# Kernel tuning notes

Measured on AMD Instinct MI355X. Metric: run time of the kernel, lower is better.

The kernel has to match this reference:

```python
import jax, jax.numpy as jnp
import numpy as np


def setup_inputs() -> dict:
    key = jax.random.key(0)
    k1, k2, k3, k4 = jax.random.split(key, 4)
    S, D, DKQ, DV = 8192, 2048, 128, 128
    x = jax.random.normal(k1, (S, D), dtype=jnp.float32)
    w_q = jax.random.uniform(k2, (D, DKQ), dtype=jnp.float32)
    w_k = jax.random.uniform(k3, (D, DKQ), dtype=jnp.float32)
    w_v = jax.random.uniform(k4, (D, DV), dtype=jnp.float32)
    return {"x": x, "w_q": w_q, "w_k": w_k, "w_v": w_v}


def reference(x, w_q, w_k, w_v):
    # x: [S, D]; single-head causal attention, unbatched as in the source.
    dim_kq = w_q.shape[1]
    q = x @ w_q  # [S, DKQ]
    k = x @ w_k  # [S, DKQ]
    v = x @ w_v  # [S, DV]
    scores = (q @ k.T) / jnp.sqrt(jnp.asarray(dim_kq, q.dtype))  # [S, S]
    S = scores.shape[0]
    causal = jnp.tril(jnp.ones((S, S), dtype=bool))
    scores = jnp.where(causal, scores, -jnp.inf)
    att_w = jax.nn.softmax(scores, axis=-1)
    return att_w @ v  # [S, DV]
```

## Files before the change

kernel.cpp:

```cpp
#include <hip/hip_runtime.h>

#define S_LEN 8192
#define D_DIM 2048
#define HD    128
#define KVB   32
#define NCH   8

typedef __attribute__((ext_vector_type(8))) short bf16x8;
typedef __attribute__((ext_vector_type(4))) float f32x4;

__device__ __forceinline__ unsigned short f2bf(float f) {
  unsigned int u = __float_as_uint(f);
  u += 0x7fffu + ((u >> 16) & 1u);
  return (unsigned short)(u >> 16);
}
__device__ __forceinline__ float bf2f(unsigned short h) {
  return __uint_as_float(((unsigned int)h) << 16);
}

__device__ __forceinline__ void glds16(const void* g, const short* l) {
  __builtin_amdgcn_global_load_lds(
      (const __attribute__((address_space(1))) void*)g,
      (__attribute__((address_space(3))) void*)l, 16, 0, 0);
}

__global__ __launch_bounds__(256)
void split_x_kernel(const float* __restrict__ x,
                    unsigned short* __restrict__ xh, unsigned short* __restrict__ xl)
{
  const size_t n4 = (size_t)S_LEN * D_DIM / 4;
  size_t idx = (size_t)blockIdx.x * 256 + threadIdx.x;
  const size_t stride = (size_t)gridDim.x * 256;
  for (; idx < n4; idx += stride) {
    float4 v = ((const float4*)x)[idx];
    ushort4 h, l;
#pragma unroll
    for (int j = 0; j < 4; ++j) {
      float f = ((const float*)&v)[j];
      unsigned short hb = f2bf(f);
      ((unsigned short*)&h)[j] = hb;
      ((unsigned short*)&l)[j] = f2bf(f - bf2f(hb));
    }
    ((ushort4*)xh)[idx] = h;
    ((ushort4*)xl)[idx] = l;
  }
}

__global__ __launch_bounds__(256)
void split_w_kernel(const float* __restrict__ wq, const float* __restrict__ wk,
                    const float* __restrict__ wv,
                    unsigned short* __restrict__ wTh, unsigned short* __restrict__ wTl)
{
  const int mode = blockIdx.y;
  const float* __restrict__ w = (mode == 0) ? wq : (mode == 1) ? wk : wv;
  unsigned short* __restrict__ oh = wTh + (size_t)mode * HD * D_DIM;
  unsigned short* __restrict__ ol = wTl + (size_t)mode * HD * D_DIM;
  const int k0 = blockIdx.x * 64;

  __shared__ float ws[64][132];
  const int t = threadIdx.x;
#pragma unroll
  for (int i = 0; i < 8; ++i) {
    int idx = t + i * 256;
    int row = idx >> 5;
    int c4  = idx & 31;
    *(float4*)&ws[row][c4 * 4] = *(const float4*)(w + (size_t)(k0 + row) * HD + c4 * 4);
  }
  __syncthreads();
#pragma unroll
  for (int i = 0; i < 4; ++i) {
    int task = t + i * 256;
    int col = task >> 3;
    int kc  = task & 7;
    ushort4 h[2], l[2];
#pragma unroll
    for (int e = 0; e < 8; ++e) {
      float f = ws[kc * 8 + e][col];
      unsigned short hb = f2bf(f);
      ((unsigned short*)&h[e >> 2])[e & 3] = hb;
      ((unsigned short*)&l[e >> 2])[e & 3] = f2bf(f - bf2f(hb));
    }
    size_t off = (size_t)col * D_DIM + k0 + kc * 8;
    *(ushort4*)(oh + off)     = h[0];
    *(ushort4*)(oh + off + 4) = h[1];
    *(ushort4*)(ol + off)     = l[0];
    *(ushort4*)(ol + off + 4) = l[1];
  }
}

__global__ __launch_bounds__(256)
void proj_kernel(const unsigned short* __restrict__ xh, const unsigned short* __restrict__ xl,
                 const unsigned short* __restrict__ wTh, const unsigned short* __restrict__ wTl,
                 unsigned short* __restrict__ q_hi, unsigned short* __restrict__ q_lo,
                 unsigned short* __restrict__ k_hi, unsigned short* __restrict__ k_lo,
                 unsigned short* __restrict__ vT)
{
  __shared__ short sm[2][12288];

  const int mode = blockIdx.y;
  const int mt   = blockIdx.x;
  const bool split = (mode < 2);

  const unsigned short* gxh = xh + (size_t)mt * 64 * D_DIM;
  const unsigned short* gxl = xl + (size_t)mt * 64 * D_DIM;
  const unsigned short* gwh = wTh + (size_t)mode * HD * D_DIM;
  const unsigned short* gwl = wTl + (size_t)mode * HD * D_DIM;

  const int t   = threadIdx.x;
  const int wid = t >> 6;
  const int ln  = t & 63;
  const int cl  = ln & 15;
  const int g4  = ln >> 4;

  auto stage = [&](int kt, int buf) {
    short* b = sm[buf];
    {
      int slot = wid * 64 + ln;
      int row = slot >> 2, sc = slot & 3;
      int kof = (sc ^ (row & 3)) * 8;
      glds16(gxh + (size_t)row * D_DIM + kt + kof, b + wid * 512);
      if (split)
        glds16(gxl + (size_t)row * D_DIM + kt + kof, b + 2048 + wid * 512);
    }
#pragma unroll
    for (int g = 0; g < 2; ++g) {
      int slot = g * 256 + wid * 64 + ln;
      int col = slot >> 2, sc = slot & 3;
      int kof = (sc ^ (col & 3)) * 8;
      glds16(gwh + (size_t)col * D_DIM + kt + kof, b + 4096 + (g * 256 + wid * 64) * 8);
      if (split)
        glds16(gwl + (size_t)col * D_DIM + kt + kof, b + 8192 + (g * 256 + wid * 64) * 8);
    }
  };

  f32x4 acc[2][4];
#pragma unroll
  for (int m = 0; m < 2; ++m)
#pragma unroll
    for (int n = 0; n < 4; ++n) acc[m][n] = f32x4{0.f, 0.f, 0.f, 0.f};

  stage(0, 0);
  __syncthreads();

  for (int kt = 0, step = 0; kt < D_DIM; kt += 32, ++step) {
    const int cur = step & 1;
    if (kt + 32 < D_DIM) stage(kt + 32, cur ^ 1);

    const short* b = sm[cur];
    bf16x8 a_h[2], a_l[2], b_h[4], b_l[4];
#pragma unroll
    for (int m = 0; m < 2; ++m) {
      int row = (wid >> 1) * 32 + m * 16 + cl;
      int byte = row * 64 + ((g4 ^ (row & 3)) << 4);
      a_h[m] = *(const bf16x8*)((const char*)b + byte);
      if (split) a_l[m] = *(const bf16x8*)((const char*)b + 4096 + byte);
    }
#pragma unroll
    for (int n = 0; n < 4; ++n) {
      int col = (wid & 1) * 64 + n * 16 + cl;
      int byte = col * 64 + ((g4 ^ (col & 3)) << 4);
      b_h[n] = *(const bf16x8*)((const char*)b + 8192 + byte);
      if (split) b_l[n] = *(const bf16x8*)((const char*)b + 16384 + byte);
    }

#pragma unroll
    for (int m = 0; m < 2; ++m)
#pragma unroll
      for (int n = 0; n < 4; ++n)
        acc[m][n] = __builtin_amdgcn_mfma_f32_16x16x32_bf16(a_h[m], b_h[n], acc[m][n], 0, 0, 0);
    if (split) {
#pragma unroll
      for (int m = 0; m < 2; ++m)
#pragma unroll
        for (int n = 0; n < 4; ++n) {
          acc[m][n] = __builtin_amdgcn_mfma_f32_16x16x32_bf16(a_l[m], b_h[n], acc[m][n], 0, 0, 0);
          acc[m][n] = __builtin_amdgcn_mfma_f32_16x16x32_bf16(a_h[m], b_l[n], acc[m][n], 0, 0, 0);
        }
    }
    __syncthreads();
  }

  const int rbase = mt * 64 + (wid >> 1) * 32 + g4 * 4;
  const int cbase = (wid & 1) * 64 + cl;

  if (mode < 2) {
    const float scale = (mode == 0) ? 0.08838834764831843f : 1.0f;
    unsigned short* __restrict__ oh = (mode == 0) ? q_hi : k_hi;
    unsigned short* __restrict__ ol = (mode == 0) ? q_lo : k_lo;
#pragma unroll
    for (int m = 0; m < 2; ++m)
#pragma unroll
      for (int n = 0; n < 4; ++n)
#pragma unroll
        for (int r = 0; r < 4; ++r) {
          float val = acc[m][n][r] * scale;
          unsigned short hb = f2bf(val);
          size_t off = (size_t)(rbase + m * 16 + r) * HD + cbase + n * 16;
          oh[off] = hb;
          ol[off] = f2bf(val - bf2f(hb));
        }
  } else {
#pragma unroll
    for (int m = 0; m < 2; ++m)
#pragma unroll
      for (int n = 0; n < 4; ++n) {
        ushort4 o;
#pragma unroll
        for (int r = 0; r < 4; ++r) ((unsigned short*)&o)[r] = f2bf(acc[m][n][r]);
        int col = cbase + n * 16;
        *(ushort4*)(vT + (size_t)col * S_LEN + rbase + m * 16) = o;
      }
  }
}

__global__ __launch_bounds__(256, 3)
void attn_kernel(const unsigned short* __restrict__ q_hi, const unsigned short* __restrict__ q_lo,
                 const unsigned short* __restrict__ k_hi, const unsigned short* __restrict__ k_lo,
                 const unsigned short* __restrict__ vT,
                 float* __restrict__ part_o, float* __restrict__ part_ml)
{
  __shared__ short ls_kh[2][4096];
  __shared__ short ls_kl[2][4096];
  __shared__ short ls_v [2][4096];
  __shared__ short ls_p [4][640];

  const int t   = threadIdx.x;
  const int wid = t >> 6;
  const int ln  = t & 63;
  const int cl  = ln & 15;
  const int g4  = ln >> 4;
  const int pairId = blockIdx.x >> 3;
  const int chunk  = blockIdx.x & 7;

  short* pw = ls_p[wid];

  auto stage = [&](int j, int buf) {
    const unsigned short* gkh = k_hi + (size_t)j * KVB * HD;
    const unsigned short* gkl = k_lo + (size_t)j * KVB * HD;
    const unsigned short* gv  = vT + (size_t)j * KVB;
#pragma unroll
    for (int i = 0; i < 2; ++i) {
      int slot = wid * 128 + i * 64 + ln;
      int row = slot >> 4, sc = slot & 15;
      int c16 = sc ^ (row & 7);
      glds16(gkh + row * HD + c16 * 8, &ls_kh[buf][(wid * 128 + i * 64) * 8]);
      glds16(gkl + row * HD + c16 * 8, &ls_kl[buf][(wid * 128 + i * 64) * 8]);
    }
#pragma unroll
    for (int i = 0; i < 2; ++i) {
      int slot = wid * 128 + i * 64 + ln;
      int d = slot >> 2, sub = slot & 3;
      int s2 = sub ^ ((d >> 1) & 3);
      glds16(gv + (size_t)d * S_LEN + s2 * 8, &ls_v[buf][(wid * 128 + i * 64) * 8]);
    }
  };

  for (int hh = 0; hh < 2; ++hh) {
    const int T = hh ? (127 - pairId) : pairId;
    const int jmaxB = T * 2 + 1;
    const int jmaxW = T * 2 + (wid >> 1);
    const int rowbase = T * 64 + wid * 16;

    bf16x8 qh[4], ql[4];
    {
      const size_t qoff = ((size_t)rowbase + cl) * HD + g4 * 8;
#pragma unroll
      for (int kc = 0; kc < 4; ++kc) {
        qh[kc] = *(const bf16x8*)(q_hi + qoff + kc * 32);
        ql[kc] = *(const bf16x8*)(q_lo + qoff + kc * 32);
      }
    }

    float m_i[4], l_i[4];
    f32x4 o_acc[8];
#pragma unroll
    for (int i = 0; i < 4; ++i) { m_i[i] = -1e30f; l_i[i] = 0.f; }
#pragma unroll
    for (int c = 0; c < 8; ++c) o_acc[c] = f32x4{0.f, 0.f, 0.f, 0.f};

    if (chunk <= jmaxB) {
      int cur = 0;
      stage(chunk, 0);
      __syncthreads();
      for (int j = chunk; j <= jmaxB; j += NCH) {
        if (j + NCH <= jmaxB) stage(j + NCH, cur ^ 1);

        if (j <= jmaxW) {
          f32x4 s[2];
          s[0] = f32x4{0.f, 0.f, 0.f, 0.f};
          s[1] = f32x4{0.f, 0.f, 0.f, 0.f};
#pragma unroll
          for (int kc = 0; kc < 4; ++kc) {
#pragma unroll
            for (int c = 0; c < 2; ++c) {
              const int kcol = c * 16 + cl;
              const int byte = kcol * 256 + ((((kc << 2) + g4) ^ (kcol & 7)) << 4);
              bf16x8 khf = *(const bf16x8*)((const char*)ls_kh[cur] + byte);
              bf16x8 klf = *(const bf16x8*)((const char*)ls_kl[cur] + byte);
              s[c] = __builtin_amdgcn_mfma_f32_16x16x32_bf16(qh[kc], khf, s[c], 0, 0, 0);
              s[c] = __builtin_amdgcn_mfma_f32_16x16x32_bf16(ql[kc], khf, s[c], 0, 0, 0);
              s[c] = __builtin_amdgcn_mfma_f32_16x16x32_bf16(qh[kc], klf, s[c], 0, 0, 0);
            }
          }

          if (j * KVB + KVB - 1 > rowbase) {
#pragma unroll
            for (int c = 0; c < 2; ++c)
#pragma unroll
              for (int i = 0; i < 4; ++i) {
                int col = j * KVB + c * 16 + cl;
                int row = rowbase + g4 * 4 + i;
                if (col > row) s[c][i] = -1e30f;
              }
          }

          bool ok = true;
#pragma unroll
          for (int i = 0; i < 4; ++i) {
            float mx = fmaxf(s[0][i], s[1][i]);
            ok = ok && (mx <= m_i[i] + 8.0f);
          }
          if (!__all(ok)) {
#pragma unroll
            for (int i = 0; i < 4; ++i) {
              float rm = fmaxf(s[0][i], s[1][i]);
              rm = fmaxf(rm, __shfl_xor(rm, 1));
              rm = fmaxf(rm, __shfl_xor(rm, 2));
              rm = fmaxf(rm, __shfl_xor(rm, 4));
              rm = fmaxf(rm, __shfl_xor(rm, 8));
              float mnew = fmaxf(m_i[i], rm);
              float corr = __expf(m_i[i] - mnew);
              l_i[i] *= corr;
#pragma unroll
              for (int c2 = 0; c2 < 8; ++c2) o_acc[c2][i] *= corr;
              m_i[i] = mnew;
            }
          }

#pragma unroll
          for (int c = 0; c < 2; ++c)
#pragma unroll
            for (int i = 0; i < 4; ++i) {
              float sv = s[c][i];
              float p = (sv > -1e29f) ? __expf(sv - m_i[i]) : 0.f;
              l_i[i] += p;
              pw[(g4 * 4 + i) * 40 + c * 16 + cl] = (short)f2bf(p);
            }

          bf16x8 pa = *(const bf16x8*)((const char*)pw + cl * 80 + g4 * 16);
#pragma unroll
          for (int c2 = 0; c2 < 8; ++c2) {
            const int d = c2 * 16 + cl;
            const int byte = d * 64 + (((g4 ^ ((d >> 1) & 3))) << 4);
            bf16x8 vb = *(const bf16x8*)((const char*)ls_v[cur] + byte);
            o_acc[c2] = __builtin_amdgcn_mfma_f32_16x16x32_bf16(pa, vb, o_acc[c2], 0, 0, 0);
          }
        }

        __syncthreads();
        cur ^= 1;
      }
    }

    const int base = T * NCH + chunk;
#pragma unroll
    for (int c2 = 0; c2 < 8; ++c2)
#pragma unroll
      for (int i = 0; i < 4; ++i)
        part_o[((size_t)base * 64 + wid * 16 + g4 * 4 + i) * HD + c2 * 16 + cl] = o_acc[c2][i];

#pragma unroll
    for (int i = 0; i < 4; ++i) {
      float lv = l_i[i];
      lv += __shfl_xor(lv, 1);
      lv += __shfl_xor(lv, 2);
      lv += __shfl_xor(lv, 4);
      lv += __shfl_xor(lv, 8);
      if (cl == 0) {
        int rl = wid * 16 + g4 * 4 + i;
        part_ml[base * 128 + rl]      = m_i[i];
        part_ml[base * 128 + 64 + rl] = lv;
      }
    }
  }
}

__global__ __launch_bounds__(128)
void merge_kernel(const float* __restrict__ part_o, const float* __restrict__ part_ml,
                  float* __restrict__ out)
{
  const int row = blockIdx.x;
  const int T   = row >> 6;
  const int r   = row & 63;
  const int c   = threadIdx.x;

  float m[NCH], l[NCH];
  float mstar = -3e38f;
#pragma unroll
  for (int s = 0; s < NCH; ++s) {
    m[s] = part_ml[(T * NCH + s) * 128 + r];
    l[s] = part_ml[(T * NCH + s) * 128 + 64 + r];
    mstar = fmaxf(mstar, m[s]);
  }
  float num = 0.f, den = 0.f;
#pragma unroll
  for (int s = 0; s < NCH; ++s) {
    float wgt = __expf(m[s] - mstar);
    den += l[s] * wgt;
    num += wgt * part_o[((size_t)(T * NCH + s) * 64 + r) * HD + c];
  }
  out[(size_t)row * HD + c] = num / den;
}

extern "C" void kernel_launch(void* const* d_in, const int* in_sizes, int n_in,
                              void* d_out, int out_size, void* d_ws, size_t ws_size,
                              hipStream_t stream)
{
  const float* x  = (const float*)d_in[0];
  const float* wq = (const float*)d_in[1];
  const float* wk = (const float*)d_in[2];
  const float* wv = (const float*)d_in[3];
  float* out = (float*)d_out;

  unsigned short* p = (unsigned short*)d_ws;
  unsigned short* xh = p;  p += (size_t)S_LEN * D_DIM;
  unsigned short* xl = p;  p += (size_t)S_LEN * D_DIM;
  unsigned short* wTh = p; p += (size_t)3 * HD * D_DIM;
  unsigned short* wTl = p; p += (size_t)3 * HD * D_DIM;
  unsigned short* q_hi = p; p += (size_t)S_LEN * HD;
  unsigned short* q_lo = p; p += (size_t)S_LEN * HD;
  unsigned short* k_hi = p; p += (size_t)S_LEN * HD;
  unsigned short* k_lo = p; p += (size_t)S_LEN * HD;
  unsigned short* vT   = p; p += (size_t)S_LEN * HD;
  float* part_o  = (float*)xh;
  float* part_ml = (float*)xl;

  split_x_kernel<<<4096, 256, 0, stream>>>(x, xh, xl);
  split_w_kernel<<<dim3(32, 3), 256, 0, stream>>>(wq, wk, wv, wTh, wTl);
  proj_kernel<<<dim3(128, 3), 256, 0, stream>>>(xh, xl, wTh, wTl,
                                                q_hi, q_lo, k_hi, k_lo, vT);
  attn_kernel<<<dim3(512), 256, 0, stream>>>(q_hi, q_lo, k_hi, k_lo, vT,
                                             part_o, part_ml);
  merge_kernel<<<dim3(8192), 128, 0, stream>>>(part_o, part_ml, out);
}
```

Before: 151.1 us.

## Switch attention to 32x32 MFMA tiles with 128-row blocks and 16 KV chunks

Restructures the attention kernel so each wave owns 32 query rows and uses 32x32x16 bf16 MFMAs instead of 16x16x32. Query tiles grow to 128 rows per block, and the KV split count rises from 8 to 16 to keep the grid size the same. Each K/V tile staged in LDS is now reused by more query rows, and fewer MFMA instructions are issued. In exchange, register pressure rises (launch bounds drop to 2 blocks per CU), the causal diagonal wastes more work, and the merge kernel must combine more partial results.

```diff
diff --git a/kernel.cpp b/kernel.cpp
--- a/kernel.cpp
+++ b/kernel.cpp
@@ -4,10 +4,11 @@
 #define D_DIM 2048
 #define HD    128
 #define KVB   32
-#define NCH   8
+#define NCH   16
 
 typedef __attribute__((ext_vector_type(8))) short bf16x8;
 typedef __attribute__((ext_vector_type(4))) float f32x4;
+typedef __attribute__((ext_vector_type(16))) float f32x16;
 
 __device__ __forceinline__ unsigned short f2bf(float f) {
   unsigned int u = __float_as_uint(f);
@@ -213,7 +214,7 @@
   }
 }
 
-__global__ __launch_bounds__(256, 3)
+__global__ __launch_bounds__(256, 2)
 void attn_kernel(const unsigned short* __restrict__ q_hi, const unsigned short* __restrict__ q_lo,
                  const unsigned short* __restrict__ k_hi, const unsigned short* __restrict__ k_lo,
                  const unsigned short* __restrict__ vT,
@@ -222,15 +223,15 @@
   __shared__ short ls_kh[2][4096];
   __shared__ short ls_kl[2][4096];
   __shared__ short ls_v [2][4096];
-  __shared__ short ls_p [4][640];
+  __shared__ short ls_p [4][32 * 40];
 
   const int t   = threadIdx.x;
   const int wid = t >> 6;
   const int ln  = t & 63;
-  const int cl  = ln & 15;
-  const int g4  = ln >> 4;
-  const int pairId = blockIdx.x >> 3;
-  const int chunk  = blockIdx.x & 7;
+  const int lc  = ln & 31;
+  const int l5  = ln >> 5;
+  const int pairId = blockIdx.x >> 4;
+  const int chunk  = blockIdx.x & 15;
 
   short* pw = ls_p[wid];
 
@@ -240,43 +241,43 @@
     const unsigned short* gv  = vT + (size_t)j * KVB;
 #pragma unroll
     for (int i = 0; i < 2; ++i) {
-      int slot = wid * 128 + i * 64 + ln;
+      int slot = i * 256 + t;
       int row = slot >> 4, sc = slot & 15;
       int c16 = sc ^ (row & 7);
-      glds16(gkh + row * HD + c16 * 8, &ls_kh[buf][(wid * 128 + i * 64) * 8]);
-      glds16(gkl + row * HD + c16 * 8, &ls_kl[buf][(wid * 128 + i * 64) * 8]);
+      glds16(gkh + row * HD + c16 * 8, &ls_kh[buf][slot * 8]);
+      glds16(gkl + row * HD + c16 * 8, &ls_kl[buf][slot * 8]);
     }
 #pragma unroll
     for (int i = 0; i < 2; ++i) {
-      int slot = wid * 128 + i * 64 + ln;
+      int slot = i * 256 + t;
       int d = slot >> 2, sub = slot & 3;
       int s2 = sub ^ ((d >> 1) & 3);
-      glds16(gv + (size_t)d * S_LEN + s2 * 8, &ls_v[buf][(wid * 128 + i * 64) * 8]);
+      glds16(gv + (size_t)d * S_LEN + s2 * 8, &ls_v[buf][slot * 8]);
     }
   };
 
   for (int hh = 0; hh < 2; ++hh) {
-    const int T = hh ? (127 - pairId) : pairId;
-    const int jmaxB = T * 2 + 1;
-    const int jmaxW = T * 2 + (wid >> 1);
-    const int rowbase = T * 64 + wid * 16;
-
-    bf16x8 qh[4], ql[4];
+    const int T = hh ? (63 - pairId) : pairId;
+    const int jmaxB = 4 * T + 3;
+    const int jmaxW = 4 * T + wid;
+    const int rowbase = T * 128 + wid * 32;
+
+    bf16x8 qh[8], ql[8];
     {
-      const size_t qoff = ((size_t)rowbase + cl) * HD + g4 * 8;
-#pragma unroll
-      for (int kc = 0; kc < 4; ++kc) {
-        qh[kc] = *(const bf16x8*)(q_hi + qoff + kc * 32);
-        ql[kc] = *(const bf16x8*)(q_lo + qoff + kc * 32);
+      const size_t qoff = ((size_t)rowbase + lc) * HD + l5 * 8;
+#pragma unroll
+      for (int ks = 0; ks < 8; ++ks) {
+        qh[ks] = *(const bf16x8*)(q_hi + qoff + ks * 16);
+        ql[ks] = *(const bf16x8*)(q_lo + qoff + ks * 16);
       }
     }
 
-    float m_i[4], l_i[4];
-    f32x4 o_acc[8];
-#pragma unroll
-    for (int i = 0; i < 4; ++i) { m_i[i] = -1e30f; l_i[i] = 0.f; }
-#pragma unroll
-    for (int c = 0; c < 8; ++c) o_acc[c] = f32x4{0.f, 0.f, 0.f, 0.f};
+    float m_i[16], l_i[16];
+    f32x16 o_acc[4];
+#pragma unroll
+    for (int r = 0; r < 16; ++r) { m_i[r] = -1e30f; l_i[r] = 0.f; }
+#pragma unroll
+    for (int ct = 0; ct < 4; ++ct) o_acc[ct] = f32x16{};
 
     if (chunk <= jmaxB) {
       int cur = 0;
@@ -286,74 +287,77 @@
         if (j + NCH <= jmaxB) stage(j + NCH, cur ^ 1);
 
         if (j <= jmaxW) {
-          f32x4 s[2];
-          s[0] = f32x4{0.f, 0.f, 0.f, 0.f};
-          s[1] = f32x4{0.f, 0.f, 0.f, 0.f};
-#pragma unroll
-          for (int kc = 0; kc < 4; ++kc) {
-#pragma unroll
-            for (int c = 0; c < 2; ++c) {
-              const int kcol = c * 16 + cl;
-              const int byte = kcol * 256 + ((((kc << 2) + g4) ^ (kcol & 7)) << 4);
-              bf16x8 khf = *(const bf16x8*)((const char*)ls_kh[cur] + byte);
-              bf16x8 klf = *(const bf16x8*)((const char*)ls_kl[cur] + byte);
-              s[c] = __builtin_amdgcn_mfma_f32_16x16x32_bf16(qh[kc], khf, s[c], 0, 0, 0);
-              s[c] = __builtin_amdgcn_mfma_f32_16x16x32_bf16(ql[kc], khf, s[c], 0, 0, 0);
-              s[c] = __builtin_amdgcn_mfma_f32_16x16x32_bf16(qh[kc], klf, s[c], 0, 0, 0);
+          f32x16 sa = f32x16{}, sb = f32x16{};
+#pragma unroll
+          for (int ks = 0; ks < 4; ++ks) {
+            const int ch = ks * 2 + l5;
+            const int byteK = lc * 256 + ((ch ^ (lc & 7)) << 4);
+            bf16x8 khf = *(const bf16x8*)((const char*)ls_kh[cur] + byteK);
+            bf16x8 klf = *(const bf16x8*)((const char*)ls_kl[cur] + byteK);
+            sa = __builtin_amdgcn_mfma_f32_32x32x16_bf16(qh[ks], khf, sa, 0, 0, 0);
+            sa = __builtin_amdgcn_mfma_f32_32x32x16_bf16(ql[ks], khf, sa, 0, 0, 0);
+            sa = __builtin_amdgcn_mfma_f32_32x32x16_bf16(qh[ks], klf, sa, 0, 0, 0);
+          }
+#pragma unroll
+          for (int ks = 4; ks < 8; ++ks) {
+            const int ch = ks * 2 + l5;
+            const int byteK = lc * 256 + ((ch ^ (lc & 7)) << 4);
+            bf16x8 khf = *(const bf16x8*)((const char*)ls_kh[cur] + byteK);
+            bf16x8 klf = *(const bf16x8*)((const char*)ls_kl[cur] + byteK);
+            sb = __builtin_amdgcn_mfma_f32_32x32x16_bf16(qh[ks], khf, sb, 0, 0, 0);
+            sb = __builtin_amdgcn_mfma_f32_32x32x16_bf16(ql[ks], khf, sb, 0, 0, 0);
+            sb = __builtin_amdgcn_mfma_f32_32x32x16_bf16(qh[ks], klf, sb, 0, 0, 0);
+          }
+          f32x16 s = sa + sb;
+
+          if (j == jmaxW) {
+#pragma unroll
+            for (int r = 0; r < 16; ++r) {
+              int row = rowbase + (r & 3) + 8 * (r >> 2) + 4 * l5;
+              int col = j * KVB + lc;
+              if (col > row) s[r] = -1e30f;
             }
           }
 
-          if (j * KVB + KVB - 1 > rowbase) {
-#pragma unroll
-            for (int c = 0; c < 2; ++c)
-#pragma unroll
-              for (int i = 0; i < 4; ++i) {
-                int col = j * KVB + c * 16 + cl;
-                int row = rowbase + g4 * 4 + i;
-                if (col > row) s[c][i] = -1e30f;
-              }
-          }
-
           bool ok = true;
 #pragma unroll
-          for (int i = 0; i < 4; ++i) {
-            float mx = fmaxf(s[0][i], s[1][i]);
-            ok = ok && (mx <= m_i[i] + 8.0f);
-          }
+          for (int r = 0; r < 16; ++r) ok = ok && (s[r] <= m_i[r] + 8.0f);
           if (!__all(ok)) {
 #pragma unroll
-            for (int i = 0; i < 4; ++i) {
-              float rm = fmaxf(s[0][i], s[1][i]);
+            for (int r = 0; r < 16; ++r) {
+              float rm = s[r];
               rm = fmaxf(rm, __shfl_xor(rm, 1));
               rm = fmaxf(rm, __shfl_xor(rm, 2));
               rm = fmaxf(rm, __shfl_xor(rm, 4));
               rm = fmaxf(rm, __shfl_xor(rm, 8));
-              float mnew = fmaxf(m_i[i], rm);
-              float corr = __expf(m_i[i] - mnew);
-              l_i[i] *= corr;
-#pragma unroll
-              for (int c2 = 0; c2 < 8; ++c2) o_acc[c2][i] *= corr;
-              m_i[i] = mnew;
+              rm = fmaxf(rm, __shfl_xor(rm, 16));
+              float mnew = fmaxf(m_i[r], rm);
+              float corr = __expf(m_i[r] - mnew);
+              l_i[r] *= corr;
+#pragma unroll
+              for (int ct = 0; ct < 4; ++ct) o_acc[ct][r] *= corr;
+              m_i[r] = mnew;
             }
           }
 
 #pragma unroll
-          for (int c = 0; c < 2; ++c)
-#pragma unroll
-            for (int i = 0; i < 4; ++i) {
-              float sv = s[c][i];
-              float p = (sv > -1e29f) ? __expf(sv - m_i[i]) : 0.f;
-              l_i[i] += p;
-              pw[(g4 * 4 + i) * 40 + c * 16 + cl] = (short)f2bf(p);
-            }
-
-          bf16x8 pa = *(const bf16x8*)((const char*)pw + cl * 80 + g4 * 16);
-#pragma unroll
-          for (int c2 = 0; c2 < 8; ++c2) {
-            const int d = c2 * 16 + cl;
-            const int byte = d * 64 + (((g4 ^ ((d >> 1) & 3))) << 4);
-            bf16x8 vb = *(const bf16x8*)((const char*)ls_v[cur] + byte);
-            o_acc[c2] = __builtin_amdgcn_mfma_f32_16x16x32_bf16(pa, vb, o_acc[c2], 0, 0, 0);
+          for (int r = 0; r < 16; ++r) {
+            float sv = s[r];
+            float p = (sv > -1e29f) ? __expf(sv - m_i[r]) : 0.f;
+            l_i[r] += p;
+            pw[((r & 3) + 8 * (r >> 2) + 4 * l5) * 40 + lc] = (short)f2bf(p);
+          }
+
+          bf16x8 pa0 = *(const bf16x8*)((const char*)pw + lc * 80 + l5 * 16);
+          bf16x8 pa1 = *(const bf16x8*)((const char*)pw + lc * 80 + 32 + l5 * 16);
+#pragma unroll
+          for (int ct = 0; ct < 4; ++ct) {
+            const int d0 = ct * 32 + lc;
+            const int sw = (d0 >> 1) & 3;
+            bf16x8 vb0 = *(const bf16x8*)((const char*)ls_v[cur] + d0 * 64 + ((l5 ^ sw) << 4));
+            bf16x8 vb1 = *(const bf16x8*)((const char*)ls_v[cur] + d0 * 64 + (((2 + l5) ^ sw) << 4));
+            o_acc[ct] = __builtin_amdgcn_mfma_f32_32x32x16_bf16(pa0, vb0, o_acc[ct], 0, 0, 0);
+            o_acc[ct] = __builtin_amdgcn_mfma_f32_32x32x16_bf16(pa1, vb1, o_acc[ct], 0, 0, 0);
           }
         }
 
@@ -364,22 +368,25 @@
 
     const int base = T * NCH + chunk;
 #pragma unroll
-    for (int c2 = 0; c2 < 8; ++c2)
-#pragma unroll
-      for (int i = 0; i < 4; ++i)
-        part_o[((size_t)base * 64 + wid * 16 + g4 * 4 + i) * HD + c2 * 16 + cl] = o_acc[c2][i];
-
-#pragma unroll
-    for (int i = 0; i < 4; ++i) {
-      float lv = l_i[i];
+    for (int ct = 0; ct < 4; ++ct)
+#pragma unroll
+      for (int r = 0; r < 16; ++r) {
+        int row = wid * 32 + (r & 3) + 8 * (r >> 2) + 4 * l5;
+        part_o[((size_t)base * 128 + row) * HD + ct * 32 + lc] = o_acc[ct][r];
+      }
+
+#pragma unroll
+    for (int r = 0; r < 16; ++r) {
+      float lv = l_i[r];
       lv += __shfl_xor(lv, 1);
       lv += __shfl_xor(lv, 2);
       lv += __shfl_xor(lv, 4);
       lv += __shfl_xor(lv, 8);
-      if (cl == 0) {
-        int rl = wid * 16 + g4 * 4 + i;
-        part_ml[base * 128 + rl]      = m_i[i];
-        part_ml[base * 128 + 64 + rl] = lv;
+      lv += __shfl_xor(lv, 16);
+      if (lc == 0) {
+        int row = wid * 32 + (r & 3) + 8 * (r >> 2) + 4 * l5;
+        part_ml[base * 256 + row]       = m_i[r];
+        part_ml[base * 256 + 128 + row] = lv;
       }
     }
   }
@@ -390,16 +397,16 @@
                   float* __restrict__ out)
 {
   const int row = blockIdx.x;
-  const int T   = row >> 6;
-  const int r   = row & 63;
+  const int T   = row >> 7;
+  const int r   = row & 127;
   const int c   = threadIdx.x;
 
   float m[NCH], l[NCH];
   float mstar = -3e38f;
 #pragma unroll
   for (int s = 0; s < NCH; ++s) {
-    m[s] = part_ml[(T * NCH + s) * 128 + r];
-    l[s] = part_ml[(T * NCH + s) * 128 + 64 + r];
+    m[s] = part_ml[(T * NCH + s) * 256 + r];
+    l[s] = part_ml[(T * NCH + s) * 256 + 128 + r];
     mstar = fmaxf(mstar, m[s]);
   }
   float num = 0.f, den = 0.f;
@@ -407,7 +414,7 @@
   for (int s = 0; s < NCH; ++s) {
     float wgt = __expf(m[s] - mstar);
     den += l[s] * wgt;
-    num += wgt * part_o[((size_t)(T * NCH + s) * 64 + r) * HD + c];
+    num += wgt * part_o[((size_t)(T * NCH + s) * 128 + r) * HD + c];
   }
   out[(size_t)row * HD + c] = num / den;
 }
@@ -433,7 +440,7 @@
   unsigned short* k_lo = p; p += (size_t)S_LEN * HD;
   unsigned short* vT   = p; p += (size_t)S_LEN * HD;
   float* part_o  = (float*)xh;
-  float* part_ml = (float*)xl;
+  float* part_ml = (float*)wTh;
 
   split_x_kernel<<<4096, 256, 0, stream>>>(x, xh, xl);
   split_w_kernel<<<dim3(32, 3), 256, 0, stream>>>(wq, wk, wv, wTh, wTl);
```

Measured after the change: 207.1 us. 1.37x slower.
